# Kernel tuning notes

Hardware: AMD Instinct MI355X
Metric: run time of the kernel (lower is better)

The kernel has to match this reference:

```python
import jax, jax.numpy as jnp
import numpy as np

B, T, W = 8, 4096, 1024          # batch, byte seq len, words per sequence
DB, DW = 64, 512                 # byte_embed_dim, word_embed_dim
NH = 2                           # highway layers per block
VOCAB = 264                      # 256 bytes + 4 + 4 specials
BPE_MARK, WORD_MARK = 4, 3       # bpe_mask_idx, word_mask_idx


def _make_seg_ids():
    # ragged word lengths in {3,4,5}, mean 4, summing to T per sequence
    rng = np.random.default_rng(0)
    seg = np.empty((B, T), np.int32)
    base = T // W
    for b in range(B):
        delta = np.zeros(W, np.int64)
        q = W // 4
        idx = rng.permutation(W)
        delta[idx[:q]] = 1
        delta[idx[q:2 * q]] = -1
        seg[b] = np.repeat(np.arange(W), base + delta)
    return jnp.asarray(seg)


def setup_inputs() -> dict:
    key = jax.random.key(0)
    ks = jax.random.split(key, 12)
    s = 0.05
    byte_tokens = jax.random.randint(ks[0], (B, T), 4, VOCAB)
    bpe_mask = jax.random.bernoulli(ks[1], 0.25, (B, T))
    word_mask = jax.random.bernoulli(ks[2], 0.05, (B, T))
    seg_ids = _make_seg_ids()
    tok_emb = (jax.random.normal(ks[3], (VOCAB, DB)) * s).at[0].set(0.0)  # padding_idx=0 row zeroed
    inp = {
        'byte_tokens': byte_tokens, 'bpe_mask': bpe_mask, 'word_mask': word_mask,
        'seg_ids': seg_ids, 'tok_emb': tok_emb,
        'conv0_w': jax.random.normal(ks[4], (3, DB, DW)) * s, 'conv0_b': jnp.zeros((DW,)),
        'hw0_wg': jax.random.normal(ks[5], (NH, DW, DW)) * s, 'hw0_bg': jnp.zeros((NH, DW)),
        'hw0_wh': jax.random.normal(ks[6], (NH, DW, DW)) * s, 'hw0_bh': jnp.zeros((NH, DW)),
        'conv1_w': jax.random.normal(ks[7], (3, DW, DW)) * s, 'conv1_b': jnp.zeros((DW,)),
        'hw1_wg': jax.random.normal(ks[8], (NH, DW, DW)) * s, 'hw1_bg': jnp.zeros((NH, DW)),
        'hw1_wh': jax.random.normal(ks[9], (NH, DW, DW)) * s, 'hw1_bh': jnp.zeros((NH, DW)),
        'proj_w': jax.random.normal(ks[10], (DW, DW)) * s, 'proj_b': jnp.zeros((DW,)),
    }
    return inp


def _conv_highway(x, cw, cb, wg, bg, wh, bh, residual):
    # 1D same-padded conv over sequence, optional residual, relu, then highways
    y = jax.lax.conv_general_dilated(x, cw, (1,), 'SAME',
                                     dimension_numbers=('NWC', 'WIO', 'NWC')) + cb
    if residual:
        y = y + x
    y = jax.nn.relu(y)
    for i in range(NH):
        g = jax.nn.sigmoid(y @ wg[i] + bg[i])
        h = jax.nn.relu(y @ wh[i] + bh[i])
        y = g * h + (1.0 - g) * y
    return y


def reference(byte_tokens, bpe_mask, word_mask, seg_ids, tok_emb,
              conv0_w, conv0_b, hw0_wg, hw0_bg, hw0_wh, hw0_bh,
              conv1_w, conv1_b, hw1_wg, hw1_bg, hw1_wh, hw1_bh,
              proj_w, proj_b):
    # byte embedding + marker embeddings (pad idx 0 -> zero row)
    x = (tok_emb[byte_tokens]
         + tok_emb[jnp.where(bpe_mask, BPE_MARK, 0)]
         + tok_emb[jnp.where(word_mask, WORD_MARK, 0)])          # [B,T,DB]
    x = _conv_highway(x, conv0_w, conv0_b, hw0_wg, hw0_bg, hw0_wh, hw0_bh, False)
    x = _conv_highway(x, conv1_w, conv1_b, hw1_wg, hw1_bg, hw1_wh, hw1_bh, True)
    # ragged per-word segment max over bytes (fused, replaces python loops)
    seg_max = jax.vmap(lambda xi, si: jax.ops.segment_max(xi, si, num_segments=W))
    x = seg_max(x, seg_ids)                                       # [B,W,DW]
    return x @ proj_w + proj_b
```

## Files before the change

### kernel.cpp

```cpp
#include <hip/hip_runtime.h>
#include <hip/hip_bf16.h>

using bf16 = __hip_bfloat16;
typedef __attribute__((ext_vector_type(8))) short s8v;
typedef __attribute__((ext_vector_type(4))) float f4v;

#define T_SEQ 4096
#define DWC 512

__device__ __forceinline__ float fin(float v) {
    return (v == v && fabsf(v) < 1e30f) ? v : 0.0f;
}
__device__ __forceinline__ float ldf(const void* p, size_t i, int f32) {
    return f32 ? ((const float*)p)[i] : __bfloat162float(((const bf16*)p)[i]);
}
__device__ __forceinline__ float b2f(short s) {
    unsigned u = ((unsigned)(unsigned short)s) << 16;
    return __builtin_bit_cast(float, u);
}
__device__ __forceinline__ short f2b(float v) {
    bf16 b = __float2bfloat16(v);
    return __builtin_bit_cast(short, b);
}

__device__ __forceinline__ void dma16(const short* g, short* l) {
    __builtin_amdgcn_global_load_lds(
        (const __attribute__((address_space(1))) void*)g,
        (__attribute__((address_space(3))) void*)l, 16, 0, 0);
}

__device__ __forceinline__ void swz(int L, int G, int& bx, int& by) {
    int k8 = L & 7, sl = L >> 3;
    int gp = G >> 5;
    bx = sl & 3;
    by = k8 * gp + (sl >> 2);
}

__device__ __forceinline__ int swidx(int row, int ch) {
    return row * 32 + ((ch ^ ((row >> 1) & 3)) << 3);
}

__global__ __launch_bounds__(256) void diag_kernel(bf16* __restrict__ out, int n, float v)
{
    int i = blockIdx.x * 256 + threadIdx.x;
    if (i < n) out[i] = __float2bfloat16(i == 0 ? v : 0.0f);
}

__global__ __launch_bounds__(256) void detect_kernel(
    const int* __restrict__ tok, const unsigned char* __restrict__ bpe,
    const unsigned char* __restrict__ wm, const int* __restrict__ seg,
    const unsigned int* __restrict__ embw, int* __restrict__ flags)
{
    __shared__ int sh[5];
    int tid = threadIdx.x;
    if (tid < 5) sh[tid] = 0;
    __syncthreads();
    int bo = 0, bm = 0, wo = 0, wmid = 0;
    for (int i = tid; i < 16384; i += 256) {
        int odd = 2 * i + 1;
        if (bpe[odd]) bo = 1;
        if (wm[odd])  wo = 1;
        int mid = 8 * (i & 4095) + 4;
        if (bpe[mid]) bm = 1;
        if (wm[mid])  wmid = 1;
    }
    if (bo)   atomicOr(&sh[0], 1);
    if (bm)   atomicOr(&sh[1], 1);
    if (wo)   atomicOr(&sh[2], 1);
    if (wmid) atomicOr(&sh[3], 1);
    if (tid < 32 && embw[32 + tid] != 0u) atomicOr(&sh[4], 1);
    __syncthreads();
    if (tid == 0) {
        flags[0] = (tok[32767] != 0) ? 0 : 1;
        flags[1] = sh[0] ? 1 : (sh[1] ? 4 : 8);
        flags[2] = sh[2] ? 1 : (sh[3] ? 4 : 8);
        flags[3] = (seg[32767] != 0) ? 0 : 1;
        flags[4] = sh[4] ? 0 : 1;
    }
}

#define WB_TOTAL 3249664
__global__ __launch_bounds__(256) void convert_weights(
    const void* c0w, const void* c0b, const void* h0g, const void* h0bg,
    const void* h0h, const void* h0bh, const void* c1w, const void* c1b,
    const void* h1g, const void* h1bg, const void* h1h, const void* h1bh,
    const void* pw, const void* pb, const int* __restrict__ flags,
    short* __restrict__ WB)
{
    int f32 = flags[4];
    size_t i = (size_t)blockIdx.x * 256 + threadIdx.x;
    if (i >= WB_TOTAL + 64) return;
    if (i >= WB_TOTAL) { WB[i] = 0; return; }
    const void* src; size_t si;
    if (i < 98304)        { size_t n = i / 192, k = i % 192; src = c0w; si = k * 512 + n; }
    else if (i < 98816)   { src = c0b;  si = i - 98304; }
    else if (i < 623104)  { size_t o = i - 98816;  size_t l = o >> 18; o &= 262143;
                            size_t n = o >> 9, k = o & 511; src = h0g; si = (l << 18) + k * 512 + n; }
    else if (i < 624128)  { src = h0bg; si = i - 623104; }
    else if (i < 1148416) { size_t o = i - 624128; size_t l = o >> 18; o &= 262143;
                            size_t n = o >> 9, k = o & 511; src = h0h; si = (l << 18) + k * 512 + n; }
    else if (i < 1149440) { src = h0bh; si = i - 1148416; }
    else if (i < 1935872) { size_t o = i - 1149440; size_t n = o / 1536, k = o % 1536;
                            src = c1w; si = k * 512 + n; }
    else if (i < 1936384) { src = c1b;  si = i - 1935872; }
    else if (i < 2460672) { size_t o = i - 1936384; size_t l = o >> 18; o &= 262143;
                            size_t n = o >> 9, k = o & 511; src = h1g; si = (l << 18) + k * 512 + n; }
    else if (i < 2461696) { src = h1bg; si = i - 2460672; }
    else if (i < 2985984) { size_t o = i - 2461696; size_t l = o >> 18; o &= 262143;
                            size_t n = o >> 9, k = o & 511; src = h1h; si = (l << 18) + k * 512 + n; }
    else if (i < 2987008) { src = h1bh; si = i - 2985984; }
    else if (i < 3249152) { size_t o = i - 2987008; size_t n = o >> 9, k = o & 511;
                            src = pw; si = k * 512 + n; }
    else                  { src = pb;   si = i - 3249152; }
    WB[i] = f2b(ldf(src, si, f32));
}

__global__ __launch_bounds__(256) void embed_kernel(
    const int* __restrict__ tok, const unsigned char* __restrict__ bpe,
    const unsigned char* __restrict__ wm, const void* __restrict__ emb,
    const int* __restrict__ flags, short* __restrict__ xe, int bt0)
{
    int i = blockIdx.x * 256 + threadIdx.x;
    int d = i & 63;
    int btl = i >> 6;
    int bt = bt0 + btl;
    int is64t = flags[0];
    int wb = flags[1], ww = flags[2];
    int f32 = flags[4];
    int t = is64t ? (int)((const long long*)tok)[bt] : tok[bt];
    t = min(max(t, 0), 263);
    float v = ldf(emb, (size_t)t * 64 + d, f32);
    if (bpe[(size_t)bt * wb]) v += ldf(emb, 4 * 64 + d, f32);
    if (wm[(size_t)bt * ww])  v += ldf(emb, 3 * 64 + d, f32);
    xe[i] = f2b(fin(v));
}

template<int IC, bool RESID>
__global__ __launch_bounds__(512) void conv_mfma(
    const short* __restrict__ A, const short* __restrict__ WT,
    const short* __restrict__ bias, const short* __restrict__ zpad,
    short* __restrict__ Out)
{
    constexpr int K = 3 * IC;
    constexpr int NIT = K / 32;
    __shared__ __align__(16) short As[2][128 * 32];
    __shared__ __align__(16) short Bs[2][128 * 32];
    int bx, by;
    swz(blockIdx.x, gridDim.x, bx, by);
    const int bm = by * 128, bn = bx * 128;
    const int tid = threadIdx.x;
    const int wave = tid >> 6, lane = tid & 63;
    const int wmr = (wave >> 1) * 32, wnc = (wave & 1) * 64;
    const int q = lane >> 4, ln16 = lane & 15;
    const int row = (wave << 4) + (lane >> 2);
    const int chl = (lane & 3) ^ ((row >> 1) & 3);
    const int gr = bm + row;
    const int tt = gr & (T_SEQ - 1);
    const short* Bbase = WT + (size_t)(bn + row) * K + chl * 8;

    f4v acc[2][4] = {};
    int p = 0;

    {
        int ts = tt - 1;
        const short* sa = (ts >= 0 && ts < T_SEQ) ? A + (size_t)(gr - 1) * IC + chl * 8 : zpad;
        dma16(sa, &As[0][wave << 9]);
        dma16(Bbase, &Bs[0][wave << 9]);
    }
    for (int it = 0; it < NIT; ++it) {
        __syncthreads();
        if (it + 1 < NIT) {
            int kn = (it + 1) * 32;
            int tap = kn / IC, c0 = kn - tap * IC;
            int ts = tt + tap - 1;
            const short* sa = (ts >= 0 && ts < T_SEQ)
                ? A + (size_t)(gr + tap - 1) * IC + c0 + chl * 8 : zpad;
            dma16(sa, &As[p ^ 1][wave << 9]);
            dma16(Bbase + kn, &Bs[p ^ 1][wave << 9]);
        }
        s8v af[2], bf[4];
        #pragma unroll
        for (int mi = 0; mi < 2; mi++) af[mi] = *(const s8v*)(&As[p][swidx(wmr + mi * 16 + ln16, q)]);
        #pragma unroll
        for (int ni = 0; ni < 4; ni++) bf[ni] = *(const s8v*)(&Bs[p][swidx(wnc + ni * 16 + ln16, q)]);
        #pragma unroll
        for (int mi = 0; mi < 2; mi++)
            #pragma unroll
            for (int ni = 0; ni < 4; ni++)
                acc[mi][ni] = __builtin_amdgcn_mfma_f32_16x16x32_bf16(
                    af[mi], bf[ni], acc[mi][ni], 0, 0, 0);
        p ^= 1;
    }

    #pragma unroll
    for (int mi = 0; mi < 2; mi++)
        #pragma unroll
        for (int ni = 0; ni < 4; ni++) {
            int col = bn + wnc + ni * 16 + ln16;
            float bv = b2f(bias[col]);
            #pragma unroll
            for (int r = 0; r < 4; r++) {
                int orow = bm + wmr + mi * 16 + q * 4 + r;
                float v = acc[mi][ni][r] + bv;
                if constexpr (RESID) v += b2f(A[(size_t)orow * IC + col]);
                Out[(size_t)orow * DWC + col] = f2b(fin(fmaxf(v, 0.0f)));
            }
        }
}

__global__ __launch_bounds__(512) void highway_mfma(
    const short* __restrict__ Y, const short* __restrict__ WgT,
    const short* __restrict__ bg, const short* __restrict__ WhT,
    const short* __restrict__ bh, short* __restrict__ Out)
{
    constexpr int NIT = DWC / 32;
    __shared__ __align__(16) short As[2][128 * 32];
    __shared__ __align__(16) short Bg[2][128 * 32];
    __shared__ __align__(16) short Bh[2][128 * 32];
    int bx, by;
    swz(blockIdx.x, gridDim.x, bx, by);
    const int bm = by * 128, bn = bx * 128;
    const int tid = threadIdx.x;
    const int wave = tid >> 6, lane = tid & 63;
    const int wmr = (wave >> 1) * 32, wnc = (wave & 1) * 64;
    const int q = lane >> 4, ln16 = lane & 15;
    const int row = (wave << 4) + (lane >> 2);
    const int chl = (lane & 3) ^ ((row >> 1) & 3);
    const short* Abase = Y   + (size_t)(bm + row) * DWC + chl * 8;
    const short* Gbase = WgT + (size_t)(bn + row) * DWC + chl * 8;
    const short* Hbase = WhT + (size_t)(bn + row) * DWC + chl * 8;

    f4v accg[2][4] = {};
    f4v acch[2][4] = {};
    int p = 0;

    dma16(Abase, &As[0][wave << 9]);
    dma16(Gbase, &Bg[0][wave << 9]);
    dma16(Hbase, &Bh[0][wave << 9]);

    for (int it = 0; it < NIT; ++it) {
        __syncthreads();
        if (it + 1 < NIT) {
            int kn = (it + 1) * 32;
            dma16(Abase + kn, &As[p ^ 1][wave << 9]);
            dma16(Gbase + kn, &Bg[p ^ 1][wave << 9]);
            dma16(Hbase + kn, &Bh[p ^ 1][wave << 9]);
        }
        s8v af[2], bgf[4], bhf[4];
        #pragma unroll
        for (int mi = 0; mi < 2; mi++) af[mi] = *(const s8v*)(&As[p][swidx(wmr + mi * 16 + ln16, q)]);
        #pragma unroll
        for (int ni = 0; ni < 4; ni++) {
            bgf[ni] = *(const s8v*)(&Bg[p][swidx(wnc + ni * 16 + ln16, q)]);
            bhf[ni] = *(const s8v*)(&Bh[p][swidx(wnc + ni * 16 + ln16, q)]);
        }
        #pragma unroll
        for (int mi = 0; mi < 2; mi++)
            #pragma unroll
            for (int ni = 0; ni < 4; ni++) {
                accg[mi][ni] = __builtin_amdgcn_mfma_f32_16x16x32_bf16(
                    af[mi], bgf[ni], accg[mi][ni], 0, 0, 0);
                acch[mi][ni] = __builtin_amdgcn_mfma_f32_16x16x32_bf16(
                    af[mi], bhf[ni], acch[mi][ni], 0, 0, 0);
            }
        p ^= 1;
    }

    #pragma unroll
    for (int mi = 0; mi < 2; mi++)
        #pragma unroll
        for (int ni = 0; ni < 4; ni++) {
            int col = bn + wnc + ni * 16 + ln16;
            float bgv = b2f(bg[col]);
            float bhv = b2f(bh[col]);
            #pragma unroll
            for (int r = 0; r < 4; r++) {
                int orow = bm + wmr + mi * 16 + q * 4 + r;
                float g = 1.0f / (1.0f + expf(-(accg[mi][ni][r] + bgv)));
                float h = fmaxf(acch[mi][ni][r] + bhv, 0.0f);
                float y = b2f(Y[(size_t)orow * DWC + col]);
                Out[(size_t)orow * DWC + col] = f2b(fin(g * h + (1.0f - g) * y));
            }
        }
}

__global__ __launch_bounds__(512) void proj_mfma(
    const short* __restrict__ A, const short* __restrict__ WT,
    const short* __restrict__ bias, const int* __restrict__ flags,
    void* __restrict__ Out, int oroff)
{
    constexpr int NIT = DWC / 32;
    __shared__ __align__(16) short As[2][128 * 32];
    __shared__ __align__(16) short Bs[2][128 * 32];
    int bx, by;
    swz(blockIdx.x, gridDim.x, bx, by);
    const int bm = by * 128, bn = bx * 128;
    const int tid = threadIdx.x;
    const int wave = tid >> 6, lane = tid & 63;
    const int wmr = (wave >> 1) * 32, wnc = (wave & 1) * 64;
    const int q = lane >> 4, ln16 = lane & 15;
    const int row = (wave << 4) + (lane >> 2);
    const int chl = (lane & 3) ^ ((row >> 1) & 3);
    const int f32 = flags[4];
    const short* Abase = A  + (size_t)(bm + row) * DWC + chl * 8;
    const short* Bbase = WT + (size_t)(bn + row) * DWC + chl * 8;

    f4v acc[2][4] = {};
    int p = 0;

    dma16(Abase, &As[0][wave << 9]);
    dma16(Bbase, &Bs[0][wave << 9]);

    for (int it = 0; it < NIT; ++it) {
        __syncthreads();
        if (it + 1 < NIT) {
            int kn = (it + 1) * 32;
            dma16(Abase + kn, &As[p ^ 1][wave << 9]);
            dma16(Bbase + kn, &Bs[p ^ 1][wave << 9]);
        }
        s8v af[2], bf[4];
        #pragma unroll
        for (int mi = 0; mi < 2; mi++) af[mi] = *(const s8v*)(&As[p][swidx(wmr + mi * 16 + ln16, q)]);
        #pragma unroll
        for (int ni = 0; ni < 4; ni++) bf[ni] = *(const s8v*)(&Bs[p][swidx(wnc + ni * 16 + ln16, q)]);
        #pragma unroll
        for (int mi = 0; mi < 2; mi++)
            #pragma unroll
            for (int ni = 0; ni < 4; ni++)
                acc[mi][ni] = __builtin_amdgcn_mfma_f32_16x16x32_bf16(
                    af[mi], bf[ni], acc[mi][ni], 0, 0, 0);
        p ^= 1;
    }

    #pragma unroll
    for (int mi = 0; mi < 2; mi++)
        #pragma unroll
        for (int ni = 0; ni < 4; ni++) {
            int col = bn + wnc + ni * 16 + ln16;
            float bv = b2f(bias[col]);
            #pragma unroll
            for (int r = 0; r < 4; r++) {
                int orow = bm + wmr + mi * 16 + q * 4 + r;
                float v = fin(acc[mi][ni][r] + bv);
                size_t oi = (size_t)(oroff + orow) * DWC + col;
                if (f32) ((float*)Out)[oi] = v;
                else     ((bf16*)Out)[oi] = __float2bfloat16(v);
            }
        }
}

__global__ __launch_bounds__(256) void bounds_kernel(
    const int* __restrict__ seg, const int* __restrict__ flags,
    int* __restrict__ wstart, int* __restrict__ wend, int bt0)
{
    int il = blockIdx.x * 256 + threadIdx.x;
    int ig = bt0 + il;
    int is64 = flags[3];
    const long long* seg64 = (const long long*)seg;
    int t = il & (T_SEQ - 1);
    int bl = il >> 12;
    int s  = (is64 ? (int)seg64[ig] : seg[ig]) & 1023;
    int sp = (t == 0)         ? -1 : ((is64 ? (int)seg64[ig - 1] : seg[ig - 1]) & 1023);
    int sn = (t == T_SEQ - 1) ? -1 : ((is64 ? (int)seg64[ig + 1] : seg[ig + 1]) & 1023);
    int bw = (bl << 10) + s;
    if (sp != s) wstart[bw] = t;
    if (sn != s) wend[bw] = t;
}

__global__ __launch_bounds__(512) void segmax_kernel(
    const short* __restrict__ Y, const int* __restrict__ wstart,
    const int* __restrict__ wend, short* __restrict__ Out)
{
    int bw = blockIdx.x;
    int d = threadIdx.x;
    int bl = bw >> 10;
    int s = wstart[bw], e = wend[bw];
    s = min(max(s, 0), T_SEQ - 1);
    e = min(max(e, s), T_SEQ - 1);
    float m = b2f(Y[(size_t)((bl << 12) + s) * DWC + d]);
    for (int t = s + 1; t <= e; ++t)
        m = fmaxf(m, b2f(Y[(size_t)((bl << 12) + t) * DWC + d]));
    Out[(size_t)bw * DWC + d] = f2b(fin(m));
}

extern "C" void kernel_launch(void* const* d_in, const int* in_sizes, int n_in,
                              void* d_out, int out_size, void* d_ws, size_t ws_size,
                              hipStream_t stream)
{
    static const int expect[19] = {32768, 32768, 32768, 32768, 16896,
                                   98304, 512, 524288, 1024, 524288, 1024,
                                   786432, 512, 524288, 1024, 524288, 1024,
                                   262144, 512};
    int bad = -1;
    if (n_in < 19) bad = 31;
    else for (int i = 0; i < 19; i++) if (in_sizes[i] != expect[i]) { bad = i; break; }
    if (bad >= 0) {
        diag_kernel<<<dim3((out_size + 255) / 256), dim3(256), 0, stream>>>(
            (bf16*)d_out, out_size, 1e35f * (float)(1 + bad));
        return;
    }

    char* ws = (char*)d_ws;
    const size_t WBREG = 8ull << 20;
    short* WB    = (short*)ws;
    int*   flags = (int*)(ws + 6500352);
    const size_t perC = 8921088 + 8192 + 64;
    int C = 8;
    while (C > 1 && WBREG + (size_t)C * perC > ws_size) C >>= 1;
    if (WBREG + (size_t)C * perC > ws_size) {
        float ws_mib = (float)((double)ws_size / 1048576.0);
        diag_kernel<<<dim3((out_size + 255) / 256), dim3(256), 0, stream>>>(
            (bf16*)d_out, out_size, 1e30f * (16.0f + ws_mib));
        return;
    }

    const int*  byte_tokens = (const int*)d_in[0];
    const unsigned char* bpe_mask = (const unsigned char*)d_in[1];
    const unsigned char* word_mask = (const unsigned char*)d_in[2];
    const int*  seg_ids     = (const int*)d_in[3];
    const void* tok_emb = d_in[4];

    detect_kernel<<<dim3(1), dim3(256), 0, stream>>>(
        byte_tokens, bpe_mask, word_mask, seg_ids,
        (const unsigned int*)tok_emb, flags);

    convert_weights<<<dim3((WB_TOTAL + 64 + 255) / 256), dim3(256), 0, stream>>>(
        d_in[5], d_in[6], d_in[7], d_in[8], d_in[9], d_in[10],
        d_in[11], d_in[12], d_in[13], d_in[14], d_in[15], d_in[16],
        d_in[17], d_in[18], flags, WB);

    short* c0wT = WB;            short* c0b  = WB + 98304;
    short* h0gT = WB + 98816;    short* h0bg = WB + 623104;
    short* h0hT = WB + 624128;   short* h0bh = WB + 1148416;
    short* c1wT = WB + 1149440;  short* c1b  = WB + 1935872;
    short* h1gT = WB + 1936384;  short* h1bg = WB + 2460672;
    short* h1hT = WB + 2461696;  short* h1bh = WB + 2985984;
    short* pwT  = WB + 2987008;  short* pb   = WB + 3249152;
    short* zpad = WB + WB_TOTAL;
    const int LOFF = 262144, LBOFF = 512;

    for (int b0 = 0; b0 < 8; b0 += C) {
        const int rows  = C * T_SEQ;
        const int words = C * 1024;
        char*  chunk  = ws + WBREG;
        short* xe     = (short*)chunk;
        short* U      = (short*)(chunk + (size_t)C * 524288);
        short* V      = (short*)(chunk + (size_t)C * (524288 + 4194304));
        int*   wstart = (int*)(chunk + (size_t)C * 8912896);
        int*   wend   = wstart + words;
        short* segout = U;

        embed_kernel<<<dim3(rows * 64 / 256), dim3(256), 0, stream>>>(
            byte_tokens, bpe_mask, word_mask, tok_emb, flags, xe, b0 * T_SEQ);

        dim3 gg(4 * (rows / 128));
        conv_mfma<64, false><<<gg, dim3(512), 0, stream>>>(xe, c0wT, c0b, zpad, U);

        highway_mfma<<<gg, dim3(512), 0, stream>>>(U, h0gT, h0bg, h0hT, h0bh, V);
        highway_mfma<<<gg, dim3(512), 0, stream>>>(V, h0gT + LOFF, h0bg + LBOFF,
                                                   h0hT + LOFF, h0bh + LBOFF, U);

        conv_mfma<512, true><<<gg, dim3(512), 0, stream>>>(U, c1wT, c1b, zpad, V);

        highway_mfma<<<gg, dim3(512), 0, stream>>>(V, h1gT, h1bg, h1hT, h1bh, U);
        highway_mfma<<<gg, dim3(512), 0, stream>>>(U, h1gT + LOFF, h1bg + LBOFF,
                                                   h1hT + LOFF, h1bh + LBOFF, V);

        bounds_kernel<<<dim3(rows / 256), dim3(256), 0, stream>>>(
            seg_ids, flags, wstart, wend, b0 * T_SEQ);

        segmax_kernel<<<dim3(words), dim3(512), 0, stream>>>(V, wstart, wend, segout);

        proj_mfma<<<dim3(4 * (words / 128)), dim3(512), 0, stream>>>(
            segout, pwT, pb, flags, d_out, b0 * 1024);
    }
}
```

Before: 495.4 us.

## Replace LDS DMA loads with register-staged prefetch and 128x64 GEMM tiles

All MFMA GEMM kernels (conv, highway, proj) drop global_load_lds DMA in favor of loading the next K-slice into registers during MFMA compute, then writing it to swizzled LDS with a single barrier per iteration. Tiles shrink from 128x128 with 512 threads to 128x64 with 256 threads, with launch_bounds(256,4), a doubled grid and an 8-wide block swizzle. This aims to overlap global latency with compute and raise occupancy. The cost is more registers and reloading the A tile across twice as many column blocks. The zero-pad buffer is removed in favor of in-register zero fill.

```diff
diff --git a/kernel.cpp b/kernel.cpp
--- a/kernel.cpp
+++ b/kernel.cpp
@@ -22,18 +22,13 @@
     bf16 b = __float2bfloat16(v);
     return __builtin_bit_cast(short, b);
 }
-
-__device__ __forceinline__ void dma16(const short* g, short* l) {
-    __builtin_amdgcn_global_load_lds(
-        (const __attribute__((address_space(1))) void*)g,
-        (__attribute__((address_space(3))) void*)l, 16, 0, 0);
-}
-
-__device__ __forceinline__ void swz(int L, int G, int& bx, int& by) {
+__device__ __forceinline__ uint4 ld16(const short* p) { return *(const uint4*)p; }
+
+__device__ __forceinline__ void swz8(int L, int G, int& bx, int& by) {
     int k8 = L & 7, sl = L >> 3;
-    int gp = G >> 5;
-    bx = sl & 3;
-    by = k8 * gp + (sl >> 2);
+    int gp = G >> 6;
+    bx = sl & 7;
+    by = k8 * gp + (sl >> 3);
 }
 
 __device__ __forceinline__ int swidx(int row, int ch) {
@@ -89,8 +84,7 @@
 {
     int f32 = flags[4];
     size_t i = (size_t)blockIdx.x * 256 + threadIdx.x;
-    if (i >= WB_TOTAL + 64) return;
-    if (i >= WB_TOTAL) { WB[i] = 0; return; }
+    if (i >= WB_TOTAL) return;
     const void* src; size_t si;
     if (i < 98304)        { size_t n = i / 192, k = i % 192; src = c0w; si = k * 512 + n; }
     else if (i < 98816)   { src = c0b;  si = i - 98304; }
@@ -136,67 +130,78 @@
 }
 
 template<int IC, bool RESID>
-__global__ __launch_bounds__(512) void conv_mfma(
+__global__ __launch_bounds__(256, 4) void conv_mfma(
     const short* __restrict__ A, const short* __restrict__ WT,
-    const short* __restrict__ bias, const short* __restrict__ zpad,
-    short* __restrict__ Out)
+    const short* __restrict__ bias, short* __restrict__ Out)
 {
     constexpr int K = 3 * IC;
     constexpr int NIT = K / 32;
     __shared__ __align__(16) short As[2][128 * 32];
-    __shared__ __align__(16) short Bs[2][128 * 32];
+    __shared__ __align__(16) short Bs[2][64 * 32];
     int bx, by;
-    swz(blockIdx.x, gridDim.x, bx, by);
-    const int bm = by * 128, bn = bx * 128;
+    swz8(blockIdx.x, gridDim.x, bx, by);
+    const int bm = by * 128, bn = bx * 64;
     const int tid = threadIdx.x;
     const int wave = tid >> 6, lane = tid & 63;
-    const int wmr = (wave >> 1) * 32, wnc = (wave & 1) * 64;
+    const int wmr = wave * 32;
     const int q = lane >> 4, ln16 = lane & 15;
-    const int row = (wave << 4) + (lane >> 2);
-    const int chl = (lane & 3) ^ ((row >> 1) & 3);
-    const int gr = bm + row;
-    const int tt = gr & (T_SEQ - 1);
-    const short* Bbase = WT + (size_t)(bn + row) * K + chl * 8;
+    const int srow = tid >> 2, ch = tid & 3;
+    const int tt0 = (bm + srow) & (T_SEQ - 1);
+    const int tt1 = (bm + srow + 64) & (T_SEQ - 1);
 
     f4v acc[2][4] = {};
+    uint4 rA0, rA1, rB;
+    const uint4 z4 = make_uint4(0, 0, 0, 0);
+
+    {
+        int t0 = tt0 - 1, t1 = tt1 - 1;
+        rA0 = (t0 >= 0 && t0 < T_SEQ) ? ld16(A + (size_t)(bm + srow - 1) * IC + ch * 8) : z4;
+        rA1 = (t1 >= 0 && t1 < T_SEQ) ? ld16(A + (size_t)(bm + srow + 63) * IC + ch * 8) : z4;
+        rB  = ld16(WT + (size_t)(bn + srow) * K + ch * 8);
+    }
+    *(uint4*)(&As[0][swidx(srow, ch)])      = rA0;
+    *(uint4*)(&As[0][swidx(srow + 64, ch)]) = rA1;
+    *(uint4*)(&Bs[0][swidx(srow, ch)])      = rB;
+    __syncthreads();
     int p = 0;
 
-    {
-        int ts = tt - 1;
-        const short* sa = (ts >= 0 && ts < T_SEQ) ? A + (size_t)(gr - 1) * IC + chl * 8 : zpad;
-        dma16(sa, &As[0][wave << 9]);
-        dma16(Bbase, &Bs[0][wave << 9]);
-    }
     for (int it = 0; it < NIT; ++it) {
-        __syncthreads();
-        if (it + 1 < NIT) {
+        const bool more = (it + 1 < NIT);
+        if (more) {
             int kn = (it + 1) * 32;
             int tap = kn / IC, c0 = kn - tap * IC;
-            int ts = tt + tap - 1;
-            const short* sa = (ts >= 0 && ts < T_SEQ)
-                ? A + (size_t)(gr + tap - 1) * IC + c0 + chl * 8 : zpad;
-            dma16(sa, &As[p ^ 1][wave << 9]);
-            dma16(Bbase + kn, &Bs[p ^ 1][wave << 9]);
+            int t0 = tt0 + tap - 1, t1 = tt1 + tap - 1;
+            rA0 = (t0 >= 0 && t0 < T_SEQ)
+                ? ld16(A + (size_t)(bm + srow + tap - 1) * IC + c0 + ch * 8) : z4;
+            rA1 = (t1 >= 0 && t1 < T_SEQ)
+                ? ld16(A + (size_t)(bm + srow + 63 + tap) * IC + c0 + ch * 8) : z4;
+            rB  = ld16(WT + (size_t)(bn + srow) * K + kn + ch * 8);
         }
         s8v af[2], bf[4];
         #pragma unroll
         for (int mi = 0; mi < 2; mi++) af[mi] = *(const s8v*)(&As[p][swidx(wmr + mi * 16 + ln16, q)]);
         #pragma unroll
-        for (int ni = 0; ni < 4; ni++) bf[ni] = *(const s8v*)(&Bs[p][swidx(wnc + ni * 16 + ln16, q)]);
+        for (int ni = 0; ni < 4; ni++) bf[ni] = *(const s8v*)(&Bs[p][swidx(ni * 16 + ln16, q)]);
         #pragma unroll
         for (int mi = 0; mi < 2; mi++)
             #pragma unroll
             for (int ni = 0; ni < 4; ni++)
                 acc[mi][ni] = __builtin_amdgcn_mfma_f32_16x16x32_bf16(
                     af[mi], bf[ni], acc[mi][ni], 0, 0, 0);
-        p ^= 1;
+        if (more) {
+            *(uint4*)(&As[p ^ 1][swidx(srow, ch)])      = rA0;
+            *(uint4*)(&As[p ^ 1][swidx(srow + 64, ch)]) = rA1;
+            *(uint4*)(&Bs[p ^ 1][swidx(srow, ch)])      = rB;
+            __syncthreads();
+            p ^= 1;
+        }
     }
 
     #pragma unroll
     for (int mi = 0; mi < 2; mi++)
         #pragma unroll
         for (int ni = 0; ni < 4; ni++) {
-            int col = bn + wnc + ni * 16 + ln16;
+            int col = bn + ni * 16 + ln16;
             float bv = b2f(bias[col]);
             #pragma unroll
             for (int r = 0; r < 4; r++) {
@@ -208,51 +213,52 @@
         }
 }
 
-__global__ __launch_bounds__(512) void highway_mfma(
+__global__ __launch_bounds__(256, 4) void highway_mfma(
     const short* __restrict__ Y, const short* __restrict__ WgT,
     const short* __restrict__ bg, const short* __restrict__ WhT,
     const short* __restrict__ bh, short* __restrict__ Out)
 {
     constexpr int NIT = DWC / 32;
     __shared__ __align__(16) short As[2][128 * 32];
-    __shared__ __align__(16) short Bg[2][128 * 32];
-    __shared__ __align__(16) short Bh[2][128 * 32];
+    __shared__ __align__(16) short Bg[2][64 * 32];
+    __shared__ __align__(16) short Bh[2][64 * 32];
     int bx, by;
-    swz(blockIdx.x, gridDim.x, bx, by);
-    const int bm = by * 128, bn = bx * 128;
+    swz8(blockIdx.x, gridDim.x, bx, by);
+    const int bm = by * 128, bn = bx * 64;
     const int tid = threadIdx.x;
     const int wave = tid >> 6, lane = tid & 63;
-    const int wmr = (wave >> 1) * 32, wnc = (wave & 1) * 64;
+    const int wmr = wave * 32;
     const int q = lane >> 4, ln16 = lane & 15;
-    const int row = (wave << 4) + (lane >> 2);
-    const int chl = (lane & 3) ^ ((row >> 1) & 3);
-    const short* Abase = Y   + (size_t)(bm + row) * DWC + chl * 8;
-    const short* Gbase = WgT + (size_t)(bn + row) * DWC + chl * 8;
-    const short* Hbase = WhT + (size_t)(bn + row) * DWC + chl * 8;
+    const int srow = tid >> 2, ch = tid & 3;
+    const short* A0 = Y   + (size_t)(bm + srow) * DWC + ch * 8;
+    const short* A1 = Y   + (size_t)(bm + srow + 64) * DWC + ch * 8;
+    const short* G0 = WgT + (size_t)(bn + srow) * DWC + ch * 8;
+    const short* H0 = WhT + (size_t)(bn + srow) * DWC + ch * 8;
 
     f4v accg[2][4] = {};
     f4v acch[2][4] = {};
+    uint4 rA0 = ld16(A0), rA1 = ld16(A1), rG = ld16(G0), rH = ld16(H0);
+    *(uint4*)(&As[0][swidx(srow, ch)])      = rA0;
+    *(uint4*)(&As[0][swidx(srow + 64, ch)]) = rA1;
+    *(uint4*)(&Bg[0][swidx(srow, ch)])      = rG;
+    *(uint4*)(&Bh[0][swidx(srow, ch)])      = rH;
+    __syncthreads();
     int p = 0;
 
-    dma16(Abase, &As[0][wave << 9]);
-    dma16(Gbase, &Bg[0][wave << 9]);
-    dma16(Hbase, &Bh[0][wave << 9]);
-
     for (int it = 0; it < NIT; ++it) {
-        __syncthreads();
-        if (it + 1 < NIT) {
+        const bool more = (it + 1 < NIT);
+        if (more) {
             int kn = (it + 1) * 32;
-            dma16(Abase + kn, &As[p ^ 1][wave << 9]);
-            dma16(Gbase + kn, &Bg[p ^ 1][wave << 9]);
-            dma16(Hbase + kn, &Bh[p ^ 1][wave << 9]);
+            rA0 = ld16(A0 + kn); rA1 = ld16(A1 + kn);
+            rG = ld16(G0 + kn);  rH = ld16(H0 + kn);
         }
         s8v af[2], bgf[4], bhf[4];
         #pragma unroll
         for (int mi = 0; mi < 2; mi++) af[mi] = *(const s8v*)(&As[p][swidx(wmr + mi * 16 + ln16, q)]);
         #pragma unroll
         for (int ni = 0; ni < 4; ni++) {
-            bgf[ni] = *(const s8v*)(&Bg[p][swidx(wnc + ni * 16 + ln16, q)]);
-            bhf[ni] = *(const s8v*)(&Bh[p][swidx(wnc + ni * 16 + ln16, q)]);
+            bgf[ni] = *(const s8v*)(&Bg[p][swidx(ni * 16 + ln16, q)]);
+            bhf[ni] = *(const s8v*)(&Bh[p][swidx(ni * 16 + ln16, q)]);
         }
         #pragma unroll
         for (int mi = 0; mi < 2; mi++)
@@ -263,14 +269,21 @@
                 acch[mi][ni] = __builtin_amdgcn_mfma_f32_16x16x32_bf16(
                     af[mi], bhf[ni], acch[mi][ni], 0, 0, 0);
             }
-        p ^= 1;
+        if (more) {
+            *(uint4*)(&As[p ^ 1][swidx(srow, ch)])      = rA0;
+            *(uint4*)(&As[p ^ 1][swidx(srow + 64, ch)]) = rA1;
+            *(uint4*)(&Bg[p ^ 1][swidx(srow, ch)])      = rG;
+            *(uint4*)(&Bh[p ^ 1][swidx(srow, ch)])      = rH;
+            __syncthreads();
+            p ^= 1;
+        }
     }
 
     #pragma unroll
     for (int mi = 0; mi < 2; mi++)
         #pragma unroll
         for (int ni = 0; ni < 4; ni++) {
-            int col = bn + wnc + ni * 16 + ln16;
+            int col = bn + ni * 16 + ln16;
             float bgv = b2f(bg[col]);
             float bhv = b2f(bh[col]);
             #pragma unroll
@@ -284,59 +297,66 @@
         }
 }
 
-__global__ __launch_bounds__(512) void proj_mfma(
+__global__ __launch_bounds__(256, 4) void proj_mfma(
     const short* __restrict__ A, const short* __restrict__ WT,
     const short* __restrict__ bias, const int* __restrict__ flags,
     void* __restrict__ Out, int oroff)
 {
     constexpr int NIT = DWC / 32;
     __shared__ __align__(16) short As[2][128 * 32];
-    __shared__ __align__(16) short Bs[2][128 * 32];
+    __shared__ __align__(16) short Bs[2][64 * 32];
     int bx, by;
-    swz(blockIdx.x, gridDim.x, bx, by);
-    const int bm = by * 128, bn = bx * 128;
+    swz8(blockIdx.x, gridDim.x, bx, by);
+    const int bm = by * 128, bn = bx * 64;
     const int tid = threadIdx.x;
     const int wave = tid >> 6, lane = tid & 63;
-    const int wmr = (wave >> 1) * 32, wnc = (wave & 1) * 64;
+    const int wmr = wave * 32;
     const int q = lane >> 4, ln16 = lane & 15;
-    const int row = (wave << 4) + (lane >> 2);
-    const int chl = (lane & 3) ^ ((row >> 1) & 3);
+    const int srow = tid >> 2, ch = tid & 3;
     const int f32 = flags[4];
-    const short* Abase = A  + (size_t)(bm + row) * DWC + chl * 8;
-    const short* Bbase = WT + (size_t)(bn + row) * DWC + chl * 8;
+    const short* A0 = A  + (size_t)(bm + srow) * DWC + ch * 8;
+    const short* A1 = A  + (size_t)(bm + srow + 64) * DWC + ch * 8;
+    const short* B0 = WT + (size_t)(bn + srow) * DWC + ch * 8;
 
     f4v acc[2][4] = {};
+    uint4 rA0 = ld16(A0), rA1 = ld16(A1), rB = ld16(B0);
+    *(uint4*)(&As[0][swidx(srow, ch)])      = rA0;
+    *(uint4*)(&As[0][swidx(srow + 64, ch)]) = rA1;
+    *(uint4*)(&Bs[0][swidx(srow, ch)])      = rB;
+    __syncthreads();
     int p = 0;
 
-    dma16(Abase, &As[0][wave << 9]);
-    dma16(Bbase, &Bs[0][wave << 9]);
-
     for (int it = 0; it < NIT; ++it) {
-        __syncthreads();
-        if (it + 1 < NIT) {
+        const bool more = (it + 1 < NIT);
+        if (more) {
             int kn = (it + 1) * 32;
-            dma16(Abase + kn, &As[p ^ 1][wave << 9]);
-            dma16(Bbase + kn, &Bs[p ^ 1][wave << 9]);
+            rA0 = ld16(A0 + kn); rA1 = ld16(A1 + kn); rB = ld16(B0 + kn);
         }
         s8v af[2], bf[4];
         #pragma unroll
         for (int mi = 0; mi < 2; mi++) af[mi] = *(const s8v*)(&As[p][swidx(wmr + mi * 16 + ln16, q)]);
         #pragma unroll
-        for (int ni = 0; ni < 4; ni++) bf[ni] = *(const s8v*)(&Bs[p][swidx(wnc + ni * 16 + ln16, q)]);
+        for (int ni = 0; ni < 4; ni++) bf[ni] = *(const s8v*)(&Bs[p][swidx(ni * 16 + ln16, q)]);
         #pragma unroll
         for (int mi = 0; mi < 2; mi++)
             #pragma unroll
             for (int ni = 0; ni < 4; ni++)
                 acc[mi][ni] = __builtin_amdgcn_mfma_f32_16x16x32_bf16(
                     af[mi], bf[ni], acc[mi][ni], 0, 0, 0);
-        p ^= 1;
+        if (more) {
+            *(uint4*)(&As[p ^ 1][swidx(srow, ch)])      = rA0;
+            *(uint4*)(&As[p ^ 1][swidx(srow + 64, ch)]) = rA1;
+            *(uint4*)(&Bs[p ^ 1][swidx(srow, ch)])      = rB;
+            __syncthreads();
+            p ^= 1;
+        }
     }
 
     #pragma unroll
     for (int mi = 0; mi < 2; mi++)
         #pragma unroll
         for (int ni = 0; ni < 4; ni++) {
-            int col = bn + wnc + ni * 16 + ln16;
+            int col = bn + ni * 16 + ln16;
             float bv = b2f(bias[col]);
             #pragma unroll
             for (int r = 0; r < 4; r++) {
@@ -424,7 +444,7 @@
         byte_tokens, bpe_mask, word_mask, seg_ids,
         (const unsigned int*)tok_emb, flags);
 
-    convert_weights<<<dim3((WB_TOTAL + 64 + 255) / 256), dim3(256), 0, stream>>>(
+    convert_weights<<<dim3((WB_TOTAL + 255) / 256), dim3(256), 0, stream>>>(
         d_in[5], d_in[6], d_in[7], d_in[8], d_in[9], d_in[10],
         d_in[11], d_in[12], d_in[13], d_in[14], d_in[15], d_in[16],
         d_in[17], d_in[18], flags, WB);
@@ -436,7 +456,6 @@
     short* h1gT = WB + 1936384;  short* h1bg = WB + 2460672;
     short* h1hT = WB + 2461696;  short* h1bh = WB + 2985984;
     short* pwT  = WB + 2987008;  short* pb   = WB + 3249152;
-    short* zpad = WB + WB_TOTAL;
     const int LOFF = 262144, LBOFF = 512;
 
     for (int b0 = 0; b0 < 8; b0 += C) {
@@ -453,17 +472,17 @@
         embed_kernel<<<dim3(rows * 64 / 256), dim3(256), 0, stream>>>(
             byte_tokens, bpe_mask, word_mask, tok_emb, flags, xe, b0 * T_SEQ);
 
-        dim3 gg(4 * (rows / 128));
-        conv_mfma<64, false><<<gg, dim3(512), 0, stream>>>(xe, c0wT, c0b, zpad, U);
-
-        highway_mfma<<<gg, dim3(512), 0, stream>>>(U, h0gT, h0bg, h0hT, h0bh, V);
-        highway_mfma<<<gg, dim3(512), 0, stream>>>(V, h0gT + LOFF, h0bg + LBOFF,
+        dim3 gg(8 * (rows / 128));
+        conv_mfma<64, false><<<gg, dim3(256), 0, stream>>>(xe, c0wT, c0b, U);
+
+        highway_mfma<<<gg, dim3(256), 0, stream>>>(U, h0gT, h0bg, h0hT, h0bh, V);
+        highway_mfma<<<gg, dim3(256), 0, stream>>>(V, h0gT + LOFF, h0bg + LBOFF,
                                                    h0hT + LOFF, h0bh + LBOFF, U);
 
-        conv_mfma<512, true><<<gg, dim3(512), 0, stream>>>(U, c1wT, c1b, zpad, V);
-
-        highway_mfma<<<gg, dim3(512), 0, stream>>>(V, h1gT, h1bg, h1hT, h1bh, U);
-        highway_mfma<<<gg, dim3(512), 0, stream>>>(U, h1gT + LOFF, h1bg + LBOFF,
+        conv_mfma<512, true><<<gg, dim3(256), 0, stream>>>(U, c1wT, c1b, V);
+
+        highway_mfma<<<gg, dim3(256), 0, stream>>>(V, h1gT, h1bg, h1hT, h1bh, U);
+        highway_mfma<<<gg, dim3(256), 0, stream>>>(U, h1gT + LOFF, h1bg + LBOFF,
                                                    h1hT + LOFF, h1bh + LBOFF, V);
 
         bounds_kernel<<<dim3(rows / 256), dim3(256), 0, stream>>>(
@@ -471,7 +490,7 @@
 
         segmax_kernel<<<dim3(words), dim3(512), 0, stream>>>(V, wstart, wend, segout);
 
-        proj_mfma<<<dim3(4 * (words / 128)), dim3(512), 0, stream>>>(
+        proj_mfma<<<dim3(8 * (words / 128)), dim3(256), 0, stream>>>(
             segout, pwT, pb, flags, d_out, b0 * 1024);
     }
 }
```

Measured after the change: 492.9 us. No clear change (-0.5%).

## Replace global_load_lds DMA with register-staged prefetch and widen conv K-step

Applied to the files above, without the earlier changes.

Switches the GEMM kernels (conv, highway, projection) from direct global-to-LDS loads to loading 16-byte chunks into registers. These are written into the swizzled double-buffered LDS after the MFMA work, with one barrier per iteration. The conv kernel also doubles its K step to 64 per iteration with larger shared buffers, halving loop iterations and barriers. The zero-pad buffer is removed in favour of register zeros. It adds register pressure and doubles conv LDS use, which may reduce occupancy.

```diff
diff --git a/kernel.cpp b/kernel.cpp
--- a/kernel.cpp
+++ b/kernel.cpp
@@ -22,12 +22,7 @@
     bf16 b = __float2bfloat16(v);
     return __builtin_bit_cast(short, b);
 }
-
-__device__ __forceinline__ void dma16(const short* g, short* l) {
-    __builtin_amdgcn_global_load_lds(
-        (const __attribute__((address_space(1))) void*)g,
-        (__attribute__((address_space(3))) void*)l, 16, 0, 0);
-}
+__device__ __forceinline__ uint4 ld16(const short* p) { return *(const uint4*)p; }
 
 __device__ __forceinline__ void swz(int L, int G, int& bx, int& by) {
     int k8 = L & 7, sl = L >> 3;
@@ -89,8 +84,7 @@
 {
     int f32 = flags[4];
     size_t i = (size_t)blockIdx.x * 256 + threadIdx.x;
-    if (i >= WB_TOTAL + 64) return;
-    if (i >= WB_TOTAL) { WB[i] = 0; return; }
+    if (i >= WB_TOTAL) return;
     const void* src; size_t si;
     if (i < 98304)        { size_t n = i / 192, k = i % 192; src = c0w; si = k * 512 + n; }
     else if (i < 98816)   { src = c0b;  si = i - 98304; }
@@ -138,13 +132,12 @@
 template<int IC, bool RESID>
 __global__ __launch_bounds__(512) void conv_mfma(
     const short* __restrict__ A, const short* __restrict__ WT,
-    const short* __restrict__ bias, const short* __restrict__ zpad,
-    short* __restrict__ Out)
+    const short* __restrict__ bias, short* __restrict__ Out)
 {
     constexpr int K = 3 * IC;
-    constexpr int NIT = K / 32;
-    __shared__ __align__(16) short As[2][128 * 32];
-    __shared__ __align__(16) short Bs[2][128 * 32];
+    constexpr int NIT = K / 64;
+    __shared__ __align__(16) short As[2][256 * 32];
+    __shared__ __align__(16) short Bs[2][256 * 32];
     int bx, by;
     swz(blockIdx.x, gridDim.x, bx, by);
     const int bm = by * 128, bn = bx * 128;
@@ -152,44 +145,67 @@
     const int wave = tid >> 6, lane = tid & 63;
     const int wmr = (wave >> 1) * 32, wnc = (wave & 1) * 64;
     const int q = lane >> 4, ln16 = lane & 15;
-    const int row = (wave << 4) + (lane >> 2);
-    const int chl = (lane & 3) ^ ((row >> 1) & 3);
-    const int gr = bm + row;
-    const int tt = gr & (T_SEQ - 1);
-    const short* Bbase = WT + (size_t)(bn + row) * K + chl * 8;
+    const int sr = tid >> 2, sch = tid & 3;
+    const int tt = (bm + sr) & (T_SEQ - 1);
+    const short* Bb = WT + (size_t)(bn + sr) * K + sch * 8;
 
     f4v acc[2][4] = {};
-    int p = 0;
+    uint4 rA0, rA1, rB0, rB1;
+    const uint4 z4 = make_uint4(0, 0, 0, 0);
 
     {
         int ts = tt - 1;
-        const short* sa = (ts >= 0 && ts < T_SEQ) ? A + (size_t)(gr - 1) * IC + chl * 8 : zpad;
-        dma16(sa, &As[0][wave << 9]);
-        dma16(Bbase, &Bs[0][wave << 9]);
-    }
+        bool ok = (ts >= 0 && ts < T_SEQ);
+        const short* sa = A + (size_t)(bm + sr - 1) * IC + sch * 8;
+        rA0 = ok ? ld16(sa) : z4;
+        rA1 = ok ? ld16(sa + 32) : z4;
+        rB0 = ld16(Bb);
+        rB1 = ld16(Bb + 32);
+    }
+    *(uint4*)(&As[0][swidx(sr, sch)])       = rA0;
+    *(uint4*)(&As[0][swidx(128 + sr, sch)]) = rA1;
+    *(uint4*)(&Bs[0][swidx(sr, sch)])       = rB0;
+    *(uint4*)(&Bs[0][swidx(128 + sr, sch)]) = rB1;
+    __syncthreads();
+    int p = 0;
+
     for (int it = 0; it < NIT; ++it) {
-        __syncthreads();
-        if (it + 1 < NIT) {
-            int kn = (it + 1) * 32;
+        const bool more = (it + 1 < NIT);
+        if (more) {
+            int kn = (it + 1) * 64;
             int tap = kn / IC, c0 = kn - tap * IC;
             int ts = tt + tap - 1;
-            const short* sa = (ts >= 0 && ts < T_SEQ)
-                ? A + (size_t)(gr + tap - 1) * IC + c0 + chl * 8 : zpad;
-            dma16(sa, &As[p ^ 1][wave << 9]);
-            dma16(Bbase + kn, &Bs[p ^ 1][wave << 9]);
-        }
-        s8v af[2], bf[4];
-        #pragma unroll
-        for (int mi = 0; mi < 2; mi++) af[mi] = *(const s8v*)(&As[p][swidx(wmr + mi * 16 + ln16, q)]);
-        #pragma unroll
-        for (int ni = 0; ni < 4; ni++) bf[ni] = *(const s8v*)(&Bs[p][swidx(wnc + ni * 16 + ln16, q)]);
-        #pragma unroll
-        for (int mi = 0; mi < 2; mi++)
+            bool ok = (ts >= 0 && ts < T_SEQ);
+            const short* sa = A + (size_t)(bm + sr + tap - 1) * IC + c0 + sch * 8;
+            rA0 = ok ? ld16(sa) : z4;
+            rA1 = ok ? ld16(sa + 32) : z4;
+            rB0 = ld16(Bb + kn);
+            rB1 = ld16(Bb + kn + 32);
+        }
+        #pragma unroll
+        for (int ks = 0; ks < 2; ks++) {
+            s8v af[2], bf[4];
+            #pragma unroll
+            for (int mi = 0; mi < 2; mi++)
+                af[mi] = *(const s8v*)(&As[p][swidx(128 * ks + wmr + mi * 16 + ln16, q)]);
             #pragma unroll
             for (int ni = 0; ni < 4; ni++)
-                acc[mi][ni] = __builtin_amdgcn_mfma_f32_16x16x32_bf16(
-                    af[mi], bf[ni], acc[mi][ni], 0, 0, 0);
-        p ^= 1;
+                bf[ni] = *(const s8v*)(&Bs[p][swidx(128 * ks + wnc + ni * 16 + ln16, q)]);
+            #pragma unroll
+            for (int mi = 0; mi < 2; mi++)
+                #pragma unroll
+                for (int ni = 0; ni < 4; ni++)
+                    acc[mi][ni] = __builtin_amdgcn_mfma_f32_16x16x32_bf16(
+                        af[mi], bf[ni], acc[mi][ni], 0, 0, 0);
+        }
+        if (more) {
+            *(uint4*)(&As[p ^ 1][swidx(sr, sch)])       = rA0;
+            *(uint4*)(&As[p ^ 1][swidx(128 + sr, sch)]) = rA1;
+            *(uint4*)(&Bs[p ^ 1][swidx(sr, sch)])       = rB0;
+            *(uint4*)(&Bs[p ^ 1][swidx(128 + sr, sch)]) = rB1;
+            __syncthreads();
+            p ^= 1;
+        }
     }
 
     #pragma unroll
@@ -224,27 +240,26 @@
     const int wave = tid >> 6, lane = tid & 63;
     const int wmr = (wave >> 1) * 32, wnc = (wave & 1) * 64;
     const int q = lane >> 4, ln16 = lane & 15;
-    const int row = (wave << 4) + (lane >> 2);
-    const int chl = (lane & 3) ^ ((row >> 1) & 3);
-    const short* Abase = Y   + (size_t)(bm + row) * DWC + chl * 8;
-    const short* Gbase = WgT + (size_t)(bn + row) * DWC + chl * 8;
-    const short* Hbase = WhT + (size_t)(bn + row) * DWC + chl * 8;
+    const int sr = tid >> 2, sch = tid & 3;
+    const int sw = swidx(sr, sch);
+    const short* A0 = Y   + (size_t)(bm + sr) * DWC + sch * 8;
+    const short* G0 = WgT + (size_t)(bn + sr) * DWC + sch * 8;
+    const short* H0 = WhT + (size_t)(bn + sr) * DWC + sch * 8;
 
     f4v accg[2][4] = {};
     f4v acch[2][4] = {};
+    uint4 rA = ld16(A0), rG = ld16(G0), rH = ld16(H0);
+    *(uint4*)(&As[0][sw]) = rA;
+    *(uint4*)(&Bg[0][sw]) = rG;
+    *(uint4*)(&Bh[0][sw]) = rH;
+    __syncthreads();
     int p = 0;
 
-    dma16(Abase, &As[0][wave << 9]);
-    dma16(Gbase, &Bg[0][wave << 9]);
-    dma16(Hbase, &Bh[0][wave << 9]);
-
     for (int it = 0; it < NIT; ++it) {
-        __syncthreads();
-        if (it + 1 < NIT) {
+        const bool more = (it + 1 < NIT);
+        if (more) {
             int kn = (it + 1) * 32;
-            dma16(Abase + kn, &As[p ^ 1][wave << 9]);
-            dma16(Gbase + kn, &Bg[p ^ 1][wave << 9]);
-            dma16(Hbase + kn, &Bh[p ^ 1][wave << 9]);
+            rA = ld16(A0 + kn); rG = ld16(G0 + kn); rH = ld16(H0 + kn);
         }
         s8v af[2], bgf[4], bhf[4];
         #pragma unroll
@@ -263,7 +278,13 @@
                 acch[mi][ni] = __builtin_amdgcn_mfma_f32_16x16x32_bf16(
                     af[mi], bhf[ni], acch[mi][ni], 0, 0, 0);
             }
-        p ^= 1;
+        if (more) {
+            *(uint4*)(&As[p ^ 1][sw]) = rA;
+            *(uint4*)(&Bg[p ^ 1][sw]) = rG;
+            *(uint4*)(&Bh[p ^ 1][sw]) = rH;
+            __syncthreads();
+            p ^= 1;
+        }
     }
 
     #pragma unroll
@@ -299,24 +320,24 @@
     const int wave = tid >> 6, lane = tid & 63;
     const int wmr = (wave >> 1) * 32, wnc = (wave & 1) * 64;
     const int q = lane >> 4, ln16 = lane & 15;
-    const int row = (wave << 4) + (lane >> 2);
-    const int chl = (lane & 3) ^ ((row >> 1) & 3);
+    const int sr = tid >> 2, sch = tid & 3;
+    const int sw = swidx(sr, sch);
     const int f32 = flags[4];
-    const short* Abase = A  + (size_t)(bm + row) * DWC + chl * 8;
-    const short* Bbase = WT + (size_t)(bn + row) * DWC + chl * 8;
+    const short* A0 = A  + (size_t)(bm + sr) * DWC + sch * 8;
+    const short* B0 = WT + (size_t)(bn + sr) * DWC + sch * 8;
 
     f4v acc[2][4] = {};
+    uint4 rA = ld16(A0), rB = ld16(B0);
+    *(uint4*)(&As[0][sw]) = rA;
+    *(uint4*)(&Bs[0][sw]) = rB;
+    __syncthreads();
     int p = 0;
 
-    dma16(Abase, &As[0][wave << 9]);
-    dma16(Bbase, &Bs[0][wave << 9]);
-
     for (int it = 0; it < NIT; ++it) {
-        __syncthreads();
-        if (it + 1 < NIT) {
+        const bool more = (it + 1 < NIT);
+        if (more) {
             int kn = (it + 1) * 32;
-            dma16(Abase + kn, &As[p ^ 1][wave << 9]);
-            dma16(Bbase + kn, &Bs[p ^ 1][wave << 9]);
+            rA = ld16(A0 + kn); rB = ld16(B0 + kn);
         }
         s8v af[2], bf[4];
         #pragma unroll
@@ -329,7 +350,12 @@
             for (int ni = 0; ni < 4; ni++)
                 acc[mi][ni] = __builtin_amdgcn_mfma_f32_16x16x32_bf16(
                     af[mi], bf[ni], acc[mi][ni], 0, 0, 0);
-        p ^= 1;
+        if (more) {
+            *(uint4*)(&As[p ^ 1][sw]) = rA;
+            *(uint4*)(&Bs[p ^ 1][sw]) = rB;
+            __syncthreads();
+            p ^= 1;
+        }
     }
 
     #pragma unroll
@@ -424,7 +450,7 @@
         byte_tokens, bpe_mask, word_mask, seg_ids,
         (const unsigned int*)tok_emb, flags);
 
-    convert_weights<<<dim3((WB_TOTAL + 64 + 255) / 256), dim3(256), 0, stream>>>(
+    convert_weights<<<dim3((WB_TOTAL + 255) / 256), dim3(256), 0, stream>>>(
         d_in[5], d_in[6], d_in[7], d_in[8], d_in[9], d_in[10],
         d_in[11], d_in[12], d_in[13], d_in[14], d_in[15], d_in[16],
         d_in[17], d_in[18], flags, WB);
@@ -436,7 +462,6 @@
     short* h1gT = WB + 1936384;  short* h1bg = WB + 2460672;
     short* h1hT = WB + 2461696;  short* h1bh = WB + 2985984;
     short* pwT  = WB + 2987008;  short* pb   = WB + 3249152;
-    short* zpad = WB + WB_TOTAL;
     const int LOFF = 262144, LBOFF = 512;
 
     for (int b0 = 0; b0 < 8; b0 += C) {
@@ -454,13 +479,13 @@
             byte_tokens, bpe_mask, word_mask, tok_emb, flags, xe, b0 * T_SEQ);
 
         dim3 gg(4 * (rows / 128));
-        conv_mfma<64, false><<<gg, dim3(512), 0, stream>>>(xe, c0wT, c0b, zpad, U);
+        conv_mfma<64, false><<<gg, dim3(512), 0, stream>>>(xe, c0wT, c0b, U);
 
         highway_mfma<<<gg, dim3(512), 0, stream>>>(U, h0gT, h0bg, h0hT, h0bh, V);
         highway_mfma<<<gg, dim3(512), 0, stream>>>(V, h0gT + LOFF, h0bg + LBOFF,
                                                    h0hT + LOFF, h0bh + LBOFF, U);
 
-        conv_mfma<512, true><<<gg, dim3(512), 0, stream>>>(U, c1wT, c1b, zpad, V);
+        conv_mfma<512, true><<<gg, dim3(512), 0, stream>>>(U, c1wT, c1b, V);
 
         highway_mfma<<<gg, dim3(512), 0, stream>>>(V, h1gT, h1bg, h1hT, h1bh, U);
         highway_mfma<<<gg, dim3(512), 0, stream>>>(U, h1gT + LOFF, h1bg + LBOFF,
```

Measured after the change: 503.7 us. Within noise of the previous version (+1.7%).
